# Optimization experiments

Hardware: AMD Instinct MI355X
Metric: run time of the kernel (lower is better)

## Reference

```python
import jax, jax.numpy as jnp
import numpy as np

N = 100001      # item_num + 1
D = 64          # hidden_units
NNZ = 3200000   # number of nonzeros in encoder_adj (avg degree ~32)


def setup_inputs() -> dict:
    key = jax.random.key(0)
    k1, k2, k3, k4 = jax.random.split(key, 4)
    row_idx = jax.random.randint(k1, (NNZ,), 0, N, dtype=jnp.int32)
    col_idx = jax.random.randint(k2, (NNZ,), 0, N, dtype=jnp.int32)
    adj_vals = jax.random.uniform(k3, (NNZ,), dtype=jnp.float32)
    emb_weight = jax.random.normal(k4, (N, D), dtype=jnp.float32)
    return {"row_idx": row_idx, "col_idx": col_idx, "adj_vals": adj_vals,
            "emb_weight": emb_weight}


def _spmm(row_idx, col_idx, vals, x):
    # COO SpMM: out[r] += vals[e] * x[col[e]]  -> [N, D]
    gathered = vals[:, None] * x[col_idx]          # [NNZ, D]
    return jax.ops.segment_sum(gathered, row_idx, num_segments=N)


def reference(row_idx, col_idx, adj_vals, emb_weight):
    e0 = emb_weight                                 # ego embeddings
    e1 = _spmm(row_idx, col_idx, adj_vals, e0)      # GCN layer 1
    e2 = _spmm(row_idx, col_idx, adj_vals, e1)      # GCN layer 2
    summed = e0 + e1 + e2                           # sum(embeds)
    return (summed, e0, e1, e2)
```

## Files before the change

kernel.cpp:

```cpp
#include <hip/hip_runtime.h>
#include <stdint.h>

#define DHID 64
#define G_BLOCKS 256
#define BMAX 512

static inline size_t align256(size_t x) { return (x + 255) & ~(size_t)255; }


__global__ void zero_i32(int* __restrict__ p, int n) {
  int i = blockIdx.x * blockDim.x + threadIdx.x;
  if (i < n) p[i] = 0;
}

__global__ void zero_f32(float* __restrict__ p, size_t n) {
  size_t i = (size_t)blockIdx.x * blockDim.x + threadIdx.x;
  if (i < n) p[i] = 0.f;
}


__global__ void a1_hist_k(const int* __restrict__ row, int* __restrict__ histGB,
                          int nnz, int B, int chunk) {
  __shared__ int h[BMAX];
  for (int i = threadIdx.x; i < B; i += blockDim.x) h[i] = 0;
  __syncthreads();
  int g = blockIdx.x;
  int s = g * chunk, e = min(nnz, s + chunk);
  for (int j = s + threadIdx.x; j < e; j += blockDim.x)
    atomicAdd(&h[row[j] >> 8], 1);
  __syncthreads();
  for (int i = threadIdx.x; i < B; i += blockDim.x)
    histGB[i * G_BLOCKS + g] = h[i];
}

__global__ void scan_gb_k(const int* __restrict__ histGB, int* __restrict__ offGB,
                          int* __restrict__ btot, int B) {
  __shared__ int wsum[4];
  int b = blockIdx.x, t = threadIdx.x, lane = t & 63, w = t >> 6;
  int v = histGB[b * G_BLOCKS + t];
  int incl = v;
#pragma unroll
  for (int off = 1; off < 64; off <<= 1) {
    int u = __shfl_up(incl, off);
    if (lane >= off) incl += u;
  }
  if (lane == 63) wsum[w] = incl;
  __syncthreads();
  int woff = 0;
  for (int w2 = 0; w2 < w; ++w2) woff += wsum[w2];
  offGB[b * G_BLOCKS + t] = woff + incl - v;
  if (t == 0) btot[b] = wsum[0] + wsum[1] + wsum[2] + wsum[3];
}

__global__ void scan_b_k(const int* __restrict__ btot, int* __restrict__ base, int B) {
  __shared__ int wsum[4];
  int t = threadIdx.x, lane = t & 63, w = t >> 6;
  int i0 = 2 * t, i1 = 2 * t + 1;
  int v0 = (i0 < B) ? btot[i0] : 0;
  int v1 = (i1 < B) ? btot[i1] : 0;
  int ps = v0 + v1, incl = ps;
#pragma unroll
  for (int off = 1; off < 64; off <<= 1) {
    int u = __shfl_up(incl, off);
    if (lane >= off) incl += u;
  }
  if (lane == 63) wsum[w] = incl;
  __syncthreads();
  int woff = 0;
  for (int w2 = 0; w2 < w; ++w2) woff += wsum[w2];
  int ex = woff + incl - ps;
  if (i0 <= B) base[i0] = ex;
  if (i1 <= B) base[i1] = ex + v0;
}

__global__ void a2_scatter_k(const int* __restrict__ row, const int* __restrict__ col,
                             const float* __restrict__ val, const int* __restrict__ base,
                             const int* __restrict__ offGB, int2* __restrict__ stage,
                             int nnz, int B, int chunk) {
  __shared__ int cur[BMAX];
  int g = blockIdx.x;
  for (int i = threadIdx.x; i < B; i += blockDim.x)
    cur[i] = base[i] + offGB[i * G_BLOCKS + g];
  __syncthreads();
  int s = g * chunk, e = min(nnz, s + chunk);
  for (int j = s + threadIdx.x; j < e; j += blockDim.x) {
    int r = row[j];
    int b = r >> 8;
    int pos = atomicAdd(&cur[b], 1);
    int2 p;
    p.x = ((r & 255) << 24) | col[j];
    p.y = __float_as_int(val[j]);
    stage[pos] = p;
  }
}


__global__ void b1_hist_k(const int2* __restrict__ stage, const int* __restrict__ base,
                          int* __restrict__ count, int n) {
  __shared__ int h[256];
  int b = blockIdx.x, t = threadIdx.x;
  h[t] = 0;
  __syncthreads();
  int s = base[b], e = base[b + 1];
  for (int j = s + t; j < e; j += 256)
    atomicAdd(&h[((unsigned)stage[j].x) >> 24], 1);
  __syncthreads();
  int r = (b << 8) + t;
  if (r < n) count[r] = h[t];
}

__global__ void b2_scatter_k(const int2* __restrict__ stage, const int* __restrict__ base,
                             const int* __restrict__ rowstart, int2* __restrict__ edges,
                             int n) {
  __shared__ int cur[256];
  int b = blockIdx.x, t = threadIdx.x;
  int r = (b << 8) + t;
  cur[t] = (r < n) ? rowstart[r] : 0;
  __syncthreads();
  int s = base[b], e = base[b + 1];
  for (int j = s + t; j < e; j += 256) {
    int2 p = stage[j];
    int rlow = ((unsigned)p.x) >> 24;
    int pos = atomicAdd(&cur[rlow], 1);
    int2 q;
    q.x = p.x & 0xFFFFFF;
    q.y = p.y;
    edges[pos] = q;
  }
}


__global__ void scan1_k(const int* __restrict__ count, int* __restrict__ bsum, int n) {
  __shared__ int lds[4];
  int base = blockIdx.x * 2048 + threadIdx.x * 8;
  int s = 0;
#pragma unroll
  for (int i = 0; i < 8; ++i) { int idx = base + i; if (idx < n) s += count[idx]; }
#pragma unroll
  for (int off = 32; off > 0; off >>= 1) s += __shfl_down(s, off);
  if ((threadIdx.x & 63) == 0) lds[threadIdx.x >> 6] = s;
  __syncthreads();
  if (threadIdx.x == 0) bsum[blockIdx.x] = lds[0] + lds[1] + lds[2] + lds[3];
}

__global__ void scan2_k(int* __restrict__ bsum, int nb, int* __restrict__ rowstart, int n) {
  int lane = threadIdx.x;
  int v = (lane < nb) ? bsum[lane] : 0;
  int incl = v;
#pragma unroll
  for (int off = 1; off < 64; off <<= 1) {
    int t = __shfl_up(incl, off);
    if (lane >= off) incl += t;
  }
  if (lane < nb) bsum[lane] = incl - v;
  if (lane == 63) rowstart[n] = incl;
}

__global__ void scan3_k(const int* __restrict__ count, const int* __restrict__ bsum,
                        int* __restrict__ rowstart, int n) {
  __shared__ int wsum[4];
  int base = blockIdx.x * 2048 + threadIdx.x * 8;
  int vals[8];
  int s = 0;
#pragma unroll
  for (int i = 0; i < 8; ++i) { int idx = base + i; vals[i] = (idx < n) ? count[idx] : 0; s += vals[i]; }
  int lane = threadIdx.x & 63, wid = threadIdx.x >> 6;
  int incl = s;
#pragma unroll
  for (int off = 1; off < 64; off <<= 1) {
    int t = __shfl_up(incl, off);
    if (lane >= off) incl += t;
  }
  if (lane == 63) wsum[wid] = incl;
  __syncthreads();
  int run = bsum[blockIdx.x] + (incl - s);
  for (int w = 0; w < wid; ++w) run += wsum[w];
#pragma unroll
  for (int i = 0; i < 8; ++i) {
    int idx = base + i;
    if (idx < n) rowstart[idx] = run;
    run += vals[i];
  }
}


__global__ void spmm_k(const int* __restrict__ rowstart, const int2* __restrict__ edges,
                       const float* __restrict__ x, float* __restrict__ y, int n) {
  int wave = (blockIdx.x * blockDim.x + threadIdx.x) >> 6;
  int lane = threadIdx.x & 63;
  if (wave >= n) return;
  int start = __builtin_amdgcn_readfirstlane(rowstart[wave]);
  int end   = __builtin_amdgcn_readfirstlane(rowstart[wave + 1]);
  float acc = 0.f;
  int k = start;
  for (; k + 8 <= end; k += 8) {
    int2 e0 = edges[k + 0], e1 = edges[k + 1], e2 = edges[k + 2], e3 = edges[k + 3];
    int2 e4 = edges[k + 4], e5 = edges[k + 5], e6 = edges[k + 6], e7 = edges[k + 7];
    float x0 = x[((size_t)e0.x << 6) + lane];
    float x1 = x[((size_t)e1.x << 6) + lane];
    float x2 = x[((size_t)e2.x << 6) + lane];
    float x3 = x[((size_t)e3.x << 6) + lane];
    float x4 = x[((size_t)e4.x << 6) + lane];
    float x5 = x[((size_t)e5.x << 6) + lane];
    float x6 = x[((size_t)e6.x << 6) + lane];
    float x7 = x[((size_t)e7.x << 6) + lane];
    acc += __int_as_float(e0.y) * x0;
    acc += __int_as_float(e1.y) * x1;
    acc += __int_as_float(e2.y) * x2;
    acc += __int_as_float(e3.y) * x3;
    acc += __int_as_float(e4.y) * x4;
    acc += __int_as_float(e5.y) * x5;
    acc += __int_as_float(e6.y) * x6;
    acc += __int_as_float(e7.y) * x7;
  }
  for (; k < end; ++k) {
    int2 e = edges[k];
    acc += __int_as_float(e.y) * x[((size_t)e.x << 6) + lane];
  }
  y[((size_t)wave << 6) + lane] = acc;
}

__global__ void spmm_fused_k(const int* __restrict__ rowstart, const int2* __restrict__ edges,
                             const float* __restrict__ e0, const float* __restrict__ e1,
                             float* __restrict__ e2, float* __restrict__ summed,
                             float* __restrict__ e0out, int n) {
  int wave = (blockIdx.x * blockDim.x + threadIdx.x) >> 6;
  int lane = threadIdx.x & 63;
  if (wave >= n) return;
  int start = __builtin_amdgcn_readfirstlane(rowstart[wave]);
  int end   = __builtin_amdgcn_readfirstlane(rowstart[wave + 1]);
  float acc = 0.f;
  int k = start;
  for (; k + 8 <= end; k += 8) {
    int2 ea = edges[k + 0], eb = edges[k + 1], ec = edges[k + 2], ed = edges[k + 3];
    int2 ee = edges[k + 4], ef = edges[k + 5], eg = edges[k + 6], eh = edges[k + 7];
    float x0 = e1[((size_t)ea.x << 6) + lane];
    float x1 = e1[((size_t)eb.x << 6) + lane];
    float x2 = e1[((size_t)ec.x << 6) + lane];
    float x3 = e1[((size_t)ed.x << 6) + lane];
    float x4 = e1[((size_t)ee.x << 6) + lane];
    float x5 = e1[((size_t)ef.x << 6) + lane];
    float x6 = e1[((size_t)eg.x << 6) + lane];
    float x7 = e1[((size_t)eh.x << 6) + lane];
    acc += __int_as_float(ea.y) * x0;
    acc += __int_as_float(eb.y) * x1;
    acc += __int_as_float(ec.y) * x2;
    acc += __int_as_float(ed.y) * x3;
    acc += __int_as_float(ee.y) * x4;
    acc += __int_as_float(ef.y) * x5;
    acc += __int_as_float(eg.y) * x6;
    acc += __int_as_float(eh.y) * x7;
  }
  for (; k < end; ++k) {
    int2 e = edges[k];
    acc += __int_as_float(e.y) * e1[((size_t)e.x << 6) + lane];
  }
  size_t o = ((size_t)wave << 6) + lane;
  float v0 = e0[o];
  float v1 = e1[o];
  e2[o] = acc;
  summed[o] = v0 + v1 + acc;
  e0out[o] = v0;
}


__global__ void spmm_atomic_k(const int* __restrict__ row, const int* __restrict__ col,
                              const float* __restrict__ val, const float* __restrict__ x,
                              float* __restrict__ y, int nnz) {
  int wave = (blockIdx.x * blockDim.x + threadIdx.x) >> 6;
  int lane = threadIdx.x & 63;
  if (wave >= nnz) return;
  int r = row[wave]; int c = col[wave]; float v = val[wave];
  atomicAdd(&y[(size_t)r * DHID + lane], v * x[(size_t)c * DHID + lane]);
}

__global__ void sum_k(const float4* __restrict__ e0, const float4* __restrict__ e1,
                      const float4* __restrict__ e2, float4* __restrict__ summed,
                      float4* __restrict__ e0out, int n4) {
  int i = blockIdx.x * blockDim.x + threadIdx.x;
  if (i < n4) {
    float4 a = e0[i], b = e1[i], c = e2[i];
    float4 s;
    s.x = a.x + b.x + c.x;
    s.y = a.y + b.y + c.y;
    s.z = a.z + b.z + c.z;
    s.w = a.w + b.w + c.w;
    summed[i] = s;
    e0out[i] = a;
  }
}

extern "C" void kernel_launch(void* const* d_in, const int* in_sizes, int n_in,
                              void* d_out, int out_size, void* d_ws, size_t ws_size,
                              hipStream_t stream) {
  const int*   row = (const int*)d_in[0];
  const int*   col = (const int*)d_in[1];
  const float* val = (const float*)d_in[2];
  const float* emb = (const float*)d_in[3];
  int nnz = in_sizes[0];
  int n   = in_sizes[3] / DHID;
  size_t ND = (size_t)n * DHID;

  float* out    = (float*)d_out;
  float* summed = out;
  float* e0o    = out + ND;
  float* e1     = out + 2 * ND;
  float* e2     = out + 3 * ND;

  int B  = (n + 255) >> 8;
  int nb = (n + 2047) / 2048;
  int chunk = (nnz + G_BLOCKS - 1) / G_BLOCKS;

  size_t o0 = 0;
  size_t count_off    = o0; o0 += align256((size_t)(n + 1) * 4);
  size_t rowstart_off = o0; o0 += align256((size_t)(n + 1) * 4);
  size_t bsum_off     = o0; o0 += align256(256 * 4);
  size_t histGB_off   = o0; o0 += align256((size_t)BMAX * G_BLOCKS * 4);
  size_t offGB_off    = o0; o0 += align256((size_t)BMAX * G_BLOCKS * 4);
  size_t btot_off     = o0; o0 += align256((size_t)BMAX * 4);
  size_t base_off     = o0; o0 += align256((size_t)(BMAX + 1) * 4);
  size_t stage_off    = o0; o0 += align256((size_t)nnz * 8);
  size_t edges_off    = o0; o0 += align256((size_t)nnz * 8);
  size_t need_sorted = o0;

  bool use_sorted = (ws_size >= need_sorted) && (B <= BMAX) && (nb <= 64) &&
                    (n < (1 << 24));

  int rb = (int)((ND + 255) / 256);
  int n4 = (int)(ND / 4);
  int sb = (n4 + 255) / 256;
  int wb = (int)(((size_t)nnz * 64 + 255) / 256);

  if (use_sorted) {
    uint8_t* w = (uint8_t*)d_ws;
    int*  count    = (int*)(w + count_off);
    int*  rowstart = (int*)(w + rowstart_off);
    int*  bsum     = (int*)(w + bsum_off);
    int*  histGB   = (int*)(w + histGB_off);
    int*  offGB    = (int*)(w + offGB_off);
    int*  btot     = (int*)(w + btot_off);
    int*  base     = (int*)(w + base_off);
    int2* stage    = (int2*)(w + stage_off);
    int2* edges    = (int2*)(w + edges_off);

    a1_hist_k<<<G_BLOCKS, 256, 0, stream>>>(row, histGB, nnz, B, chunk);
    scan_gb_k<<<B, 256, 0, stream>>>(histGB, offGB, btot, B);
    scan_b_k<<<1, 256, 0, stream>>>(btot, base, B);
    a2_scatter_k<<<G_BLOCKS, 256, 0, stream>>>(row, col, val, base, offGB, stage,
                                               nnz, B, chunk);
    b1_hist_k<<<B, 256, 0, stream>>>(stage, base, count, n);
    scan1_k<<<nb, 256, 0, stream>>>(count, bsum, n);
    scan2_k<<<1, 64, 0, stream>>>(bsum, nb, rowstart, n);
    scan3_k<<<nb, 256, 0, stream>>>(count, bsum, rowstart, n);
    b2_scatter_k<<<B, 256, 0, stream>>>(stage, base, rowstart, edges, n);

    spmm_k<<<rb, 256, 0, stream>>>(rowstart, edges, emb, e1, n);
    spmm_fused_k<<<rb, 256, 0, stream>>>(rowstart, edges, emb, e1, e2, summed, e0o, n);
  } else {
    zero_f32<<<(int)((ND + 255) / 256), 256, 0, stream>>>(e1, ND);
    spmm_atomic_k<<<wb, 256, 0, stream>>>(row, col, val, emb, e1, nnz);
    zero_f32<<<(int)((ND + 255) / 256), 256, 0, stream>>>(e2, ND);
    spmm_atomic_k<<<wb, 256, 0, stream>>>(row, col, val, e1, e2, nnz);
    sum_k<<<sb, 256, 0, stream>>>((const float4*)emb, (const float4*)e1,
                                  (const float4*)e2, (float4*)summed,
                                  (float4*)e0o, n4);
  }
}
```

Before: 487.6 us.

## Split bucket sort passes into sub-blocks and sort edges within each row

Doubles the number of first-pass histogram blocks and splits the second-level histogram and scatter across SB sub-blocks per bucket, using a per-sub-block histogram to compute each sub-block's starting offsets. This adds parallelism to bucket passes that previously ran one block per bucket. It also adds a wave-level bitonic sort of each row's edges by column index (for rows of degree up to 64), likely aimed at gather locality or a deterministic summation order. The sort is an extra full read and write of the edge array.

```diff
diff --git a/kernel.cpp b/kernel.cpp
--- a/kernel.cpp
+++ b/kernel.cpp
@@ -2,8 +2,9 @@
 #include <stdint.h>
 
 #define DHID 64
-#define G_BLOCKS 256
+#define G_BLOCKS 512
 #define BMAX 512
+#define SB 4
 
 static inline size_t align256(size_t x) { return (x + 255) & ~(size_t)255; }
 
@@ -37,8 +38,9 @@
                           int* __restrict__ btot, int B) {
   __shared__ int wsum[4];
   int b = blockIdx.x, t = threadIdx.x, lane = t & 63, w = t >> 6;
-  int v = histGB[b * G_BLOCKS + t];
-  int incl = v;
+  int v0 = histGB[b * G_BLOCKS + 2 * t];
+  int v1 = histGB[b * G_BLOCKS + 2 * t + 1];
+  int ps = v0 + v1, incl = ps;
 #pragma unroll
   for (int off = 1; off < 64; off <<= 1) {
     int u = __shfl_up(incl, off);
@@ -48,7 +50,11 @@
   __syncthreads();
   int woff = 0;
   for (int w2 = 0; w2 < w; ++w2) woff += wsum[w2];
-  offGB[b * G_BLOCKS + t] = woff + incl - v;
+  int ex = woff + incl - ps;
+  offGB[b * G_BLOCKS + 2 * t] = ex;
+  offGB[b * G_BLOCKS + 2 * t + 1] = ex + v0;
+  if (t == 0) btot[b] = 0;
+  __syncthreads();
   if (t == 0) btot[b] = wsum[0] + wsum[1] + wsum[2] + wsum[3];
 }
 
@@ -96,29 +102,41 @@
 
 
 __global__ void b1_hist_k(const int2* __restrict__ stage, const int* __restrict__ base,
-                          int* __restrict__ count, int n) {
+                          int* __restrict__ histBS, int* __restrict__ count, int n) {
   __shared__ int h[256];
-  int b = blockIdx.x, t = threadIdx.x;
+  int b = blockIdx.x, s = blockIdx.y, t = threadIdx.x;
   h[t] = 0;
   __syncthreads();
-  int s = base[b], e = base[b + 1];
-  for (int j = s + t; j < e; j += 256)
+  int bs = base[b], be = base[b + 1];
+  int len = be - bs;
+  int sub = (len + SB - 1) / SB;
+  int s0 = bs + s * sub;
+  int s1 = min(be, s0 + sub);
+  for (int j = s0 + t; j < s1; j += 256)
     atomicAdd(&h[((unsigned)stage[j].x) >> 24], 1);
   __syncthreads();
-  int r = (b << 8) + t;
-  if (r < n) count[r] = h[t];
+  histBS[(size_t)s * BMAX * 256 + (b << 8) + t] = h[t];
+  int g = (b << 8) + t;
+  if (g < n && h[t]) atomicAdd(&count[g], h[t]);
 }
 
 __global__ void b2_scatter_k(const int2* __restrict__ stage, const int* __restrict__ base,
-                             const int* __restrict__ rowstart, int2* __restrict__ edges,
-                             int n) {
+                             const int* __restrict__ rowstart, const int* __restrict__ histBS,
+                             int2* __restrict__ edges, int n) {
   __shared__ int cur[256];
-  int b = blockIdx.x, t = threadIdx.x;
-  int r = (b << 8) + t;
-  cur[t] = (r < n) ? rowstart[r] : 0;
-  __syncthreads();
-  int s = base[b], e = base[b + 1];
-  for (int j = s + t; j < e; j += 256) {
+  int b = blockIdx.x, s = blockIdx.y, t = threadIdx.x;
+  int g = (b << 8) + t;
+  int c = (g < n) ? rowstart[g] : 0;
+  for (int s2 = 0; s2 < s; ++s2)
+    c += histBS[(size_t)s2 * BMAX * 256 + (b << 8) + t];
+  cur[t] = c;
+  __syncthreads();
+  int bs = base[b], be = base[b + 1];
+  int len = be - bs;
+  int sub = (len + SB - 1) / SB;
+  int s0 = bs + s * sub;
+  int s1 = min(be, s0 + sub);
+  for (int j = s0 + t; j < s1; j += 256) {
     int2 p = stage[j];
     int rlow = ((unsigned)p.x) >> 24;
     int pos = atomicAdd(&cur[rlow], 1);
@@ -181,6 +199,33 @@
     if (idx < n) rowstart[idx] = run;
     run += vals[i];
   }
+}
+
+
+__global__ void rowsort_k(const int* __restrict__ rowstart, int2* __restrict__ edges, int n) {
+  int wave = (blockIdx.x * blockDim.x + threadIdx.x) >> 6;
+  int lane = threadIdx.x & 63;
+  if (wave >= n) return;
+  int start = __builtin_amdgcn_readfirstlane(rowstart[wave]);
+  int end   = __builtin_amdgcn_readfirstlane(rowstart[wave + 1]);
+  int deg = end - start;
+  if (deg <= 1 || deg > 64) return;
+  int key = 0x7FFFFFFF, pay = 0;
+  if (lane < deg) { int2 e = edges[start + lane]; key = e.x; pay = e.y; }
+#pragma unroll
+  for (int k = 2; k <= 64; k <<= 1) {
+#pragma unroll
+    for (int j = k >> 1; j > 0; j >>= 1) {
+      int pk = __shfl_xor(key, j);
+      int pp = __shfl_xor(pay, j);
+      bool dir = (lane & k) == 0;
+      bool lower = (lane & j) == 0;
+      bool keepMin = (lower == dir);
+      bool take = keepMin ? (pk < key) : (pk > key);
+      if (take) { key = pk; pay = pp; }
+    }
+  }
+  if (lane < deg) { int2 q; q.x = key; q.y = pay; edges[start + lane] = q; }
 }
 
 
@@ -319,6 +364,7 @@
   size_t offGB_off    = o0; o0 += align256((size_t)BMAX * G_BLOCKS * 4);
   size_t btot_off     = o0; o0 += align256((size_t)BMAX * 4);
   size_t base_off     = o0; o0 += align256((size_t)(BMAX + 1) * 4);
+  size_t histBS_off   = o0; o0 += align256((size_t)SB * BMAX * 256 * 4);
   size_t stage_off    = o0; o0 += align256((size_t)nnz * 8);
   size_t edges_off    = o0; o0 += align256((size_t)nnz * 8);
   size_t need_sorted = o0;
@@ -340,6 +386,7 @@
     int*  offGB    = (int*)(w + offGB_off);
     int*  btot     = (int*)(w + btot_off);
     int*  base     = (int*)(w + base_off);
+    int*  histBS   = (int*)(w + histBS_off);
     int2* stage    = (int2*)(w + stage_off);
     int2* edges    = (int2*)(w + edges_off);
 
@@ -348,12 +395,14 @@
     scan_b_k<<<1, 256, 0, stream>>>(btot, base, B);
     a2_scatter_k<<<G_BLOCKS, 256, 0, stream>>>(row, col, val, base, offGB, stage,
                                                nnz, B, chunk);
-    b1_hist_k<<<B, 256, 0, stream>>>(stage, base, count, n);
+    zero_i32<<<(n + 255) / 256, 256, 0, stream>>>(count, n);
+    b1_hist_k<<<dim3(B, SB), 256, 0, stream>>>(stage, base, histBS, count, n);
     scan1_k<<<nb, 256, 0, stream>>>(count, bsum, n);
     scan2_k<<<1, 64, 0, stream>>>(bsum, nb, rowstart, n);
     scan3_k<<<nb, 256, 0, stream>>>(count, bsum, rowstart, n);
-    b2_scatter_k<<<B, 256, 0, stream>>>(stage, base, rowstart, edges, n);
-
+    b2_scatter_k<<<dim3(B, SB), 256, 0, stream>>>(stage, base, rowstart, histBS, edges, n);
+
+    rowsort_k<<<rb, 256, 0, stream>>>(rowstart, edges, n);
     spmm_k<<<rb, 256, 0, stream>>>(rowstart, edges, emb, e1, n);
     spmm_fused_k<<<rb, 256, 0, stream>>>(rowstart, edges, emb, e1, e2, summed, e0o, n);
   } else {
```

Result: slower. 523.9 us (+7.4%).
